# Optimization experiments

Measured on AMD Instinct MI355X. Metric: run time of the kernel, lower is better.

Reference implementation:

```python
import jax, jax.numpy as jnp
import numpy as np

MAX_LEN = 1024

def _make_pe():
    # matches TemporalPositionalEncoding buffer construction
    pe = np.zeros(MAX_LEN, np.float32)
    pos = np.arange(MAX_LEN, dtype=np.float64)
    d = MAX_LEN + 1e-9
    pe[0::2] = np.sin(pos[0::2] / 10000.0 ** (pos[0::2] / d))
    pe[1::2] = np.cos(pos[1::2] / 10000.0 ** (pos[1::2] / d))
    return jnp.asarray(pe, jnp.float32)


def setup_inputs() -> dict:
    key = jax.random.key(0)
    k1, k2, k3, k4, k5 = jax.random.split(key, 5)
    B, H, W, C = 16, 56, 56, 768
    sw = 4
    x = jax.random.normal(k1, (B, H, W, C), dtype=jnp.float32)
    # source inits these to zero; use small random weights so the op is non-trivial
    qkv_w = jax.random.normal(k2, (3 * sw, sw), dtype=jnp.float32) * 0.1
    qkv_b = jax.random.normal(k3, (3 * sw,), dtype=jnp.float32) * 0.1
    proj_w = jax.random.normal(k4, (C, C), dtype=jnp.float32) * 0.02
    proj_b = jax.random.normal(k5, (C,), dtype=jnp.float32) * 0.02
    pe = _make_pe()
    return {"x": x, "qkv_w": qkv_w, "qkv_b": qkv_b,
            "proj_w": proj_w, "proj_b": proj_b, "pe": pe}


def reference(x, qkv_w, qkv_b, proj_w, proj_b, pe):
    B, H, W, C = x.shape
    sw = qkv_w.shape[0] // 3  # group_size
    # temporal positional encoding along channel dim
    x = x + pe[:C].astype(x.dtype).reshape(1, 1, 1, -1)
    pad = (-C) % sw  # static Python int
    if pad:
        x = jnp.pad(x, ((0, 0), (0, 0), (0, 0), (0, pad)))
    Cp = x.shape[-1]
    N = Cp // sw
    xg = x.reshape(B * H * W, N, sw)  # [G, N, sw]
    qkv = xg @ qkv_w.T + qkv_b        # [G, N, 3*sw]
    q, k, v = jnp.split(qkv, 3, axis=-1)
    # SDPA with q,k,v of shape [G, N, 1, sw]: seq length (L=S=1) attention.
    # softmax over the single key is identically 1, so out == v; we keep the
    # explicit score/softmax for structural fidelity (it's scalar-per-group).
    scale = 1.0 / jnp.sqrt(jnp.asarray(sw, x.dtype))
    scores = jnp.einsum('gnd,gnd->gn', q, k) * scale          # [G, N]
    attn = jax.nn.softmax(scores[..., None, None], axis=-1)   # [G, N, 1, 1] == 1
    out = attn[..., 0] * v                                    # [G, N, sw]
    out = out.reshape(B, H, W, Cp)[..., :C]
    return out @ proj_w.T + proj_b
```

## Files before the change

kernel.cpp:

```cpp
#include <hip/hip_runtime.h>
#include <hip/hip_bf16.h>

typedef __attribute__((ext_vector_type(8))) short bf16x8;
typedef __attribute__((ext_vector_type(4))) float f32x4;
typedef __attribute__((ext_vector_type(4))) unsigned short u16x4;
typedef unsigned short u16;

#define M_DIM 50176
#define N_DIM 768
#define K_DIM 768

__device__ __forceinline__ u16 f2bf(float f) {
    __hip_bfloat16 h = __float2bfloat16(f);
    return *reinterpret_cast<u16*>(&h);
}

__device__ __forceinline__ void gld_lds16(const void* g, void* l) {
    __builtin_amdgcn_global_load_lds(
        (const __attribute__((address_space(1))) unsigned int*)g,
        (__attribute__((address_space(3))) unsigned int*)l, 16, 0, 0);
}

__global__ void fold_weights(const float* __restrict__ qkv_w,
                             const float* __restrict__ qkv_b,
                             const float* __restrict__ proj_w,
                             const float* __restrict__ proj_b,
                             const float* __restrict__ pe,
                             u16* __restrict__ Bw, float* __restrict__ bias) {
    const int o = blockIdx.x;
    const int t = threadIdx.x;
    __shared__ float wv[16];
    __shared__ float bv4[4];
    __shared__ float red[4];
    if (t < 16) wv[t] = qkv_w[32 + t];
    if (t < 4)  bv4[t] = qkv_b[8 + t];
    __syncthreads();
    const float* Prow = proj_w + o * 768;
    float s = 0.f;
    for (int c = t; c < 768; c += 256) {
        int g4 = c & ~3, j = c & 3;
        float af = Prow[g4 + 0] * wv[0 * 4 + j] + Prow[g4 + 1] * wv[1 * 4 + j] +
                   Prow[g4 + 2] * wv[2 * 4 + j] + Prow[g4 + 3] * wv[3 * 4 + j];
        Bw[o * 768 + c] = f2bf(af);
        s += af * pe[c];
        s += Prow[c] * bv4[j];
    }
    #pragma unroll
    for (int off = 32; off; off >>= 1) s += __shfl_down(s, off, 64);
    if ((t & 63) == 0) red[t >> 6] = s;
    __syncthreads();
    if (t == 0) bias[o] = red[0] + red[1] + red[2] + red[3] + proj_b[o];
}

__global__ __launch_bounds__(256, 2)
void gemm_fused(const float* __restrict__ X, const u16* __restrict__ Bw,
                const float* __restrict__ bias, float* __restrict__ Y) {
    const int b = blockIdx.x;
    const int bid = (b & 7) * 294 + (b >> 3);
    const int mt = bid / 6, nt = bid - mt * 6;
    const int m0 = mt * 128, n0 = nt * 128;

    const int tid = threadIdx.x;
    const int lane = tid & 63;
    const int w = tid >> 6;
    const int wm = w >> 1, wn = w & 1;

    __shared__ u16 As[2][128 * 64];
    __shared__ u16 Bs[2][128 * 64];

    f32x4 acc[4][4];
    #pragma unroll
    for (int i = 0; i < 4; ++i)
        #pragma unroll
        for (int j = 0; j < 4; ++j)
            acc[i][j] = (f32x4){0.f, 0.f, 0.f, 0.f};

    const int arow = tid >> 4;
    const int agg  = tid & 15;
    const int bg = lane & 7;

    float4 preA[8], preB[8];

    auto load_a = [&](float4 (&p)[8], int k0) {
        const float4* src = (const float4*)(X + (long)m0 * K_DIM + k0);
        #pragma unroll
        for (int i = 0; i < 8; ++i) {
            int r = arow + 16 * i;
            p[i] = src[(long)r * (K_DIM / 4) + agg];
        }
    };

    auto write_a = [&](int buf, const float4 (&p)[8]) {
        #pragma unroll
        for (int i = 0; i < 8; ++i) {
            int r = arow + 16 * i;
            int pb = (agg * 8) ^ ((r & 7) << 4);
            u16x4 hv;
            hv.x = f2bf(p[i].x);
            hv.y = f2bf(p[i].y);
            hv.z = f2bf(p[i].z);
            hv.w = f2bf(p[i].w);
            *(u16x4*)&As[buf][r * 64 + (pb >> 1)] = hv;
        }
    };

    auto stage_b = [&](int buf, int k0) {
        #pragma unroll
        for (int j = 0; j < 4; ++j) {
            int rowbase = j * 32 + w * 8;
            int row = rowbase + (lane >> 3);
            const char* src = (const char*)Bw + ((long)(n0 + row) * K_DIM + k0) * 2 +
                              ((bg * 16) ^ ((row & 7) << 4));
            gld_lds16(src, (void*)&Bs[buf][rowbase * 64]);
        }
    };

    auto compute = [&](int buf) {
        #pragma unroll
        for (int h = 0; h < 2; ++h) {
            bf16x8 av[4], bv_[4];
            #pragma unroll
            for (int mf = 0; mf < 4; ++mf) {
                int r = wm * 64 + mf * 16 + (lane & 15);
                int pb = (h * 64 + ((lane >> 4) << 4)) ^ ((r & 7) << 4);
                av[mf] = *(const bf16x8*)&As[buf][r * 64 + (pb >> 1)];
            }
            #pragma unroll
            for (int nf = 0; nf < 4; ++nf) {
                int r = wn * 64 + nf * 16 + (lane & 15);
                int pb = (h * 64 + ((lane >> 4) << 4)) ^ ((r & 7) << 4);
                bv_[nf] = *(const bf16x8*)&Bs[buf][r * 64 + (pb >> 1)];
            }
            __builtin_amdgcn_s_setprio(1);
            #pragma unroll
            for (int mf = 0; mf < 4; ++mf)
                #pragma unroll
                for (int nf = 0; nf < 4; ++nf)
                    acc[mf][nf] = __builtin_amdgcn_mfma_f32_16x16x32_bf16(
                        av[mf], bv_[nf], acc[mf][nf], 0, 0, 0);
            __builtin_amdgcn_s_setprio(0);
        }
    };

    load_a(preA, 0);
    stage_b(0, 0);
    load_a(preB, 64);
    write_a(0, preA);
    __syncthreads();

    const int NT = K_DIM / 64;
    #pragma unroll 1
    for (int t2 = 0; t2 < NT; t2 += 2) {
        if (t2 + 1 < NT) {
            write_a(1, preB);
            stage_b(1, (t2 + 1) * 64);
        }
        if (t2 + 2 < NT) load_a(preA, (t2 + 2) * 64);
        compute(0);
        __syncthreads();

        if (t2 + 2 < NT) {
            write_a(0, preA);
            stage_b(0, (t2 + 2) * 64);
        }
        if (t2 + 3 < NT) load_a(preB, (t2 + 3) * 64);
        compute(1);
        __syncthreads();
    }

    const int colq = lane & 15;
    const int rowq = (lane >> 4) * 4;
    #pragma unroll
    for (int nf = 0; nf < 4; ++nf) {
        int col = n0 + wn * 64 + nf * 16 + colq;
        float bi = bias[col];
        #pragma unroll
        for (int mf = 0; mf < 4; ++mf) {
            long rbase = m0 + wm * 64 + mf * 16 + rowq;
            #pragma unroll
            for (int r = 0; r < 4; ++r) {
                __builtin_nontemporal_store(acc[mf][nf][r] + bi,
                                            &Y[(rbase + r) * N_DIM + col]);
            }
        }
    }
}

extern "C" void kernel_launch(void* const* d_in, const int* in_sizes, int n_in,
                              void* d_out, int out_size, void* d_ws, size_t ws_size,
                              hipStream_t stream) {
    const float* x      = (const float*)d_in[0];
    const float* qkv_w  = (const float*)d_in[1];
    const float* qkv_b  = (const float*)d_in[2];
    const float* proj_w = (const float*)d_in[3];
    const float* proj_b = (const float*)d_in[4];
    const float* pe     = (const float*)d_in[5];
    float* y = (float*)d_out;

    u16*   Bw   = (u16*)d_ws;
    float* bias = (float*)((char*)d_ws + (size_t)N_DIM * K_DIM * 2);

    fold_weights<<<768, 256, 0, stream>>>(qkv_w, qkv_b, proj_w, proj_b, pe, Bw, bias);
    gemm_fused<<<(M_DIM / 128) * (N_DIM / 128), 256, 0, stream>>>(x, Bw, bias, y);
}
```

Baseline: 104.9 us.

## Pre-convert X to bf16 in a separate pass and use a global-to-LDS GEMM

Adds a kernel that converts the fp32 activation matrix to bf16 in workspace. A new GEMM then stages both A and B tiles directly into LDS with global_load_lds, single-buffered, at higher occupancy. This removes the in-loop fp32 load and convert work and halves the bytes of A re-read across N tiles. The cost is a full extra read and write pass over X through HBM, plus a large workspace requirement; the old path is kept as a fallback.

```diff
diff --git a/kernel.cpp b/kernel.cpp
--- a/kernel.cpp
+++ b/kernel.cpp
@@ -9,6 +9,7 @@
 #define M_DIM 50176
 #define N_DIM 768
 #define K_DIM 768
+#define XB_ELEMS ((size_t)M_DIM * K_DIM)
 
 __device__ __forceinline__ u16 f2bf(float f) {
     __hip_bfloat16 h = __float2bfloat16(f);
@@ -19,6 +20,22 @@
     __builtin_amdgcn_global_load_lds(
         (const __attribute__((address_space(1))) unsigned int*)g,
         (__attribute__((address_space(3))) unsigned int*)l, 16, 0, 0);
+}
+
+__global__ __launch_bounds__(256)
+void cvt_x(const float* __restrict__ X, u16* __restrict__ Xb) {
+    const size_t n8 = XB_ELEMS / 8;
+    for (size_t i = (size_t)blockIdx.x * blockDim.x + threadIdx.x; i < n8;
+         i += (size_t)gridDim.x * blockDim.x) {
+        const float4* src = (const float4*)(X + i * 8);
+        float4 a = src[0], b = src[1];
+        u16x4 lo, hi;
+        lo.x = f2bf(a.x); lo.y = f2bf(a.y); lo.z = f2bf(a.z); lo.w = f2bf(a.w);
+        hi.x = f2bf(b.x); hi.y = f2bf(b.y); hi.z = f2bf(b.z); hi.w = f2bf(b.w);
+        u16x4* dst = (u16x4*)(Xb + i * 8);
+        dst[0] = lo;
+        dst[1] = hi;
+    }
 }
 
 __global__ void fold_weights(const float* __restrict__ qkv_w,
@@ -52,6 +69,105 @@
     if (t == 0) bias[o] = red[0] + red[1] + red[2] + red[3] + proj_b[o];
 }
 
+__global__ __launch_bounds__(256, 4)
+void gemm_bf16(const u16* __restrict__ Xb, const u16* __restrict__ Bw,
+               const float* __restrict__ bias, float* __restrict__ Y) {
+    const int b = blockIdx.x;
+    const int bid = (b & 7) * 294 + (b >> 3);
+    const int mt = bid / 6, nt = bid - mt * 6;
+    const int m0 = mt * 128, n0 = nt * 128;
+
+    const int tid = threadIdx.x;
+    const int lane = tid & 63;
+    const int w = tid >> 6;
+    const int wm = w >> 1, wn = w & 1;
+
+    __shared__ u16 As[128 * 64];
+    __shared__ u16 Bs[128 * 64];
+
+    f32x4 acc[4][4];
+    #pragma unroll
+    for (int i = 0; i < 4; ++i)
+        #pragma unroll
+        for (int j = 0; j < 4; ++j)
+            acc[i][j] = (f32x4){0.f, 0.f, 0.f, 0.f};
+
+    const int bg = lane & 7;
+
+    auto stage = [&](const u16* srcbase, u16* lds, int k0) {
+        #pragma unroll
+        for (int j = 0; j < 4; ++j) {
+            int rowbase = j * 32 + w * 8;
+            int row = rowbase + (lane >> 3);
+            const char* src = (const char*)srcbase + ((long)row * K_DIM + k0) * 2 +
+                              ((bg * 16) ^ ((row & 7) << 4));
+            gld_lds16(src, (void*)&lds[rowbase * 64]);
+        }
+    };
+
+    auto compute = [&]() {
+        #pragma unroll
+        for (int h = 0; h < 2; ++h) {
+            bf16x8 av[4], bv_[4];
+            #pragma unroll
+            for (int mf = 0; mf < 4; ++mf) {
+                int r = wm * 64 + mf * 16 + (lane & 15);
+                int pb = (h * 64 + ((lane >> 4) << 4)) ^ ((r & 7) << 4);
+                av[mf] = *(const bf16x8*)&As[r * 64 + (pb >> 1)];
+            }
+            #pragma unroll
+            for (int nf = 0; nf < 4; ++nf) {
+                int r = wn * 64 + nf * 16 + (lane & 15);
+                int pb = (h * 64 + ((lane >> 4) << 4)) ^ ((r & 7) << 4);
+                bv_[nf] = *(const bf16x8*)&Bs[r * 64 + (pb >> 1)];
+            }
+            __builtin_amdgcn_s_setprio(1);
+            #pragma unroll
+            for (int mf = 0; mf < 4; ++mf)
+                #pragma unroll
+                for (int nf = 0; nf < 4; ++nf)
+                    acc[mf][nf] = __builtin_amdgcn_mfma_f32_16x16x32_bf16(
+                        av[mf], bv_[nf], acc[mf][nf], 0, 0, 0);
+            __builtin_amdgcn_s_setprio(0);
+        }
+    };
+
+    const u16* Abase = Xb + (long)m0 * K_DIM;
+    const u16* Bbase = Bw + (long)n0 * K_DIM;
+
+    stage(Abase, As, 0);
+    stage(Bbase, Bs, 0);
+    __syncthreads();
+
+    const int NT = K_DIM / 64;
+    #pragma unroll 1
+    for (int t = 0; t < NT - 1; ++t) {
+        compute();
+        __syncthreads();
+        stage(Abase, As, (t + 1) * 64);
+        stage(Bbase, Bs, (t + 1) * 64);
+        __syncthreads();
+    }
+    compute();
+
+    const int colq = lane & 15;
+    const int rowq = (lane >> 4) * 4;
+    #pragma unroll
+    for (int nf = 0; nf < 4; ++nf) {
+        int col = n0 + wn * 64 + nf * 16 + colq;
+        float bi = bias[col];
+        #pragma unroll
+        for (int mf = 0; mf < 4; ++mf) {
+            long rbase = m0 + wm * 64 + mf * 16 + rowq;
+            #pragma unroll
+            for (int r = 0; r < 4; ++r) {
+                __builtin_nontemporal_store(acc[mf][nf][r] + bi,
+                                            &Y[(rbase + r) * N_DIM + col]);
+            }
+        }
+    }
+}
+
 __global__ __launch_bounds__(256, 2)
 void gemm_fused(const float* __restrict__ X, const u16* __restrict__ Bw,
                 const float* __restrict__ bias, float* __restrict__ Y) {
@@ -197,9 +313,21 @@
     const float* pe     = (const float*)d_in[5];
     float* y = (float*)d_out;
 
-    u16*   Bw   = (u16*)d_ws;
-    float* bias = (float*)((char*)d_ws + (size_t)N_DIM * K_DIM * 2);
-
-    fold_weights<<<768, 256, 0, stream>>>(qkv_w, qkv_b, proj_w, proj_b, pe, Bw, bias);
-    gemm_fused<<<(M_DIM / 128) * (N_DIM / 128), 256, 0, stream>>>(x, Bw, bias, y);
-}
+    const size_t xb_bytes   = XB_ELEMS * 2;
+    const size_t bw_bytes   = (size_t)N_DIM * K_DIM * 2;
+    const size_t bias_bytes = N_DIM * sizeof(float);
+
+    if (ws_size >= xb_bytes + bw_bytes + bias_bytes) {
+        u16*   Xb   = (u16*)d_ws;
+        u16*   Bw   = (u16*)((char*)d_ws + xb_bytes);
+        float* bias = (float*)((char*)d_ws + xb_bytes + bw_bytes);
+        fold_weights<<<768, 256, 0, stream>>>(qkv_w, qkv_b, proj_w, proj_b, pe, Bw, bias);
+        cvt_x<<<2048, 256, 0, stream>>>(x, Xb);
+        gemm_bf16<<<(M_DIM / 128) * (N_DIM / 128), 256, 0, stream>>>(Xb, Bw, bias, y);
+    } else {
+        u16*   Bw   = (u16*)d_ws;
+        float* bias = (float*)((char*)d_ws + bw_bytes);
+        fold_weights<<<768, 256, 0, stream>>>(qkv_w, qkv_b, proj_w, proj_b, pe, Bw, bias);
+        gemm_fused<<<(M_DIM / 128) * (N_DIM / 128), 256, 0, stream>>>(x, Bw, bias, y);
+    }
+}
```

After: 117.6 us. 1.12x slower.
